# Performance work log

Hardware: AMD Instinct MI355X
Metric: run time of the kernel (lower is better)

## Reference

```python
import jax, jax.numpy as jnp
import numpy as np

B, T, H = 2, 2048, 1024
NH = 16
HD = H // NH


def setup_inputs() -> dict:
    key = jax.random.key(0)
    ks = jax.random.split(key, 9)
    s = 0.02
    return {
        "x": jax.random.normal(ks[0], (B, T, H), dtype=jnp.float32),
        "attn_mask": jnp.ones((B, T), dtype=jnp.int32),
        "Wq": jax.random.normal(ks[1], (H, H), dtype=jnp.float32) * s,
        "bq": jnp.zeros((H,), dtype=jnp.float32),
        "Wk": jax.random.normal(ks[2], (H, H), dtype=jnp.float32) * s,
        "bk": jnp.zeros((H,), dtype=jnp.float32),
        "Wv": jax.random.normal(ks[3], (H, H), dtype=jnp.float32) * s,
        "bv": jnp.zeros((H,), dtype=jnp.float32),
        "Wo": jax.random.normal(ks[4], (H, H), dtype=jnp.float32) * s,
        "bo": jnp.zeros((H,), dtype=jnp.float32),
    }


def reference(x, attn_mask, Wq, bq, Wk, bk, Wv, bv, Wo, bo):
    Bc, Tc, Hc = x.shape
    scale = HD ** -0.5
    # projections; torch Linear: y = x @ W.T + b (here W stored as [in,out])
    q = (x @ Wq + bq).reshape(Bc, Tc, NH, HD).transpose(0, 2, 1, 3)  # [B,NH,T,HD]
    k = (x @ Wk + bk).reshape(Bc, Tc, NH, HD).transpose(0, 2, 1, 3)
    v = (x @ Wv + bv).reshape(Bc, Tc, NH, HD).transpose(0, 2, 1, 3)
    scores = jnp.einsum('bhqd,bhkd->bhqk', q, k) * scale  # [B,NH,T,T]
    mask = attn_mask.reshape(Bc, 1, 1, Tc)
    scores = jnp.where(mask == 0, jnp.float32(-jnp.inf), scores)
    probs = jax.nn.softmax(scores, axis=-1)
    ctx = jnp.einsum('bhqk,bhkd->bhqd', probs, v)  # [B,NH,T,HD]
    ctx = ctx.transpose(0, 2, 1, 3).reshape(Bc, Tc, Hc)
    out = ctx @ Wo + bo
    return out
```

## Files before the change

kernel.cpp:

```cpp
#include <hip/hip_runtime.h>

typedef _Float16 f16;
typedef _Float16 f16x8 __attribute__((ext_vector_type(8)));
typedef _Float16 f16x4 __attribute__((ext_vector_type(4)));
typedef __fp16 h16x2 __attribute__((ext_vector_type(2)));
typedef float f32x4 __attribute__((ext_vector_type(4)));

#define MFMA32(a, b, c) __builtin_amdgcn_mfma_f32_16x16x32_f16((a), (b), (c), 0, 0, 0)
#define MFMA16(a, b, c) __builtin_amdgcn_mfma_f32_16x16x16f16((a), (b), (c), 0, 0, 0)

static constexpr int Bb = 2, T = 2048, H = 1024, NH = 16, HD = 64;
static constexpr int M = Bb * T;
static constexpr int NQKV = 3 * H;
#define QSCALE 0.1803368801111f

__device__ __forceinline__ void gload_lds16(const void* g, void* l) {
  __builtin_amdgcn_global_load_lds(
      (const __attribute__((address_space(1))) void*)g,
      (__attribute__((address_space(3))) void*)l, 16, 0, 0);
}

__global__ __launch_bounds__(256) void pack_all(const float* __restrict__ x,
                                                const float* __restrict__ Wq,
                                                const float* __restrict__ Wk,
                                                const float* __restrict__ Wv,
                                                const float* __restrict__ Wo,
                                                const float* __restrict__ bq,
                                                const float* __restrict__ bk,
                                                const float* __restrict__ bv,
                                                f16* __restrict__ xh,
                                                f16* __restrict__ WqkvT,
                                                f16* __restrict__ WoT,
                                                float* __restrict__ bqkv) {
  __shared__ f16 tile[64][65];
  const int bid = blockIdx.x;
  if (bid < 4096) {
    int i = bid * 256 + threadIdx.x;
    float4 v = ((const float4*)x)[i];
    f16x4 o;
    o[0] = (f16)v.x; o[1] = (f16)v.y; o[2] = (f16)v.z; o[3] = (f16)v.w;
    *(f16x4*)(xh + (size_t)i * 4) = o;
  } else if (bid < 5120) {
    int t = bid - 4096;
    int z = t >> 8, rem = t & 255;
    const float* W = (z == 0) ? Wq : (z == 1) ? Wk : (z == 2) ? Wv : Wo;
    f16* Wt = (z < 3) ? (WqkvT + (size_t)z * H * H) : WoT;
    const float scale = (z == 0) ? QSCALE : 1.0f;
    int k0 = (rem >> 4) * 64, n0 = (rem & 15) * 64;
    for (int p = 0; p < 16; ++p) {
      int idx = threadIdx.x + p * 256;
      int r = idx >> 6, c = idx & 63;
      tile[r][c] = (f16)(W[(size_t)(k0 + r) * H + n0 + c] * scale);
    }
    __syncthreads();
    for (int p = 0; p < 16; ++p) {
      int idx = threadIdx.x + p * 256;
      int r = idx >> 6, c = idx & 63;
      Wt[(size_t)(n0 + r) * H + k0 + c] = tile[c][r];
    }
  } else {
    int i = (bid - 5120) * 256 + threadIdx.x;
    if (i < 3072) {
      float v = (i < 1024) ? bq[i] * QSCALE : ((i < 2048) ? bk[i - 1024] : bv[i - 2048]);
      bqkv[i] = v;
    }
  }
}

__device__ __forceinline__ f16x8 lds_frag(const f16* base, int row, int gr) {
  return *(const f16x8*)(base + row * 64 + ((gr ^ (row & 7)) << 3));
}

template <int TM, int TN, bool OUT_F32>
__global__ __launch_bounds__(256) void gemm_f16_bt(const f16* __restrict__ A,
                                                   const f16* __restrict__ Bt,
                                                   const float* __restrict__ bias,
                                                   void* __restrict__ Cout,
                                                   int Nn, int Kk) {
  __shared__ f16 As[TM * 64];
  __shared__ f16 Bs[TN * 64];
  const int tid = threadIdx.x;
  const int lane = tid & 63, w = tid >> 6;
  const int quad = lane >> 4, l16 = lane & 15;
  const int wm = w >> 1, wn = w & 1;
  const int m0 = blockIdx.y * TM, n0 = blockIdx.x * TN;
  constexpr int AM = TM / 32, AN = TN / 32;

  f32x4 acc[AM][AN];
  for (int a = 0; a < AM; ++a)
    for (int b2 = 0; b2 < AN; ++b2)
      for (int r = 0; r < 4; ++r) acc[a][b2][r] = 0.f;

  for (int k0 = 0; k0 < Kk; k0 += 64) {
    for (int p = 0; p < TM * 8 / 256; ++p) {
      int slot = p * 256 + w * 64 + lane;
      int r = slot >> 3, g = (slot & 7) ^ (r & 7);
      gload_lds16(A + (size_t)(m0 + r) * Kk + k0 + g * 8,
                  (char*)As + (p * 256 + w * 64) * 16);
    }
    for (int p = 0; p < TN * 8 / 256; ++p) {
      int slot = p * 256 + w * 64 + lane;
      int r = slot >> 3, g = (slot & 7) ^ (r & 7);
      gload_lds16(Bt + (size_t)(n0 + r) * Kk + k0 + g * 8,
                  (char*)Bs + (p * 256 + w * 64) * 16);
    }
    __syncthreads();
    for (int ks = 0; ks < 2; ++ks) {
      f16x8 af[AM], bf[AN];
      for (int t = 0; t < AM; ++t)
        af[t] = lds_frag(As, wm * (TM / 2) + t * 16 + l16, ks * 4 + quad);
      for (int t = 0; t < AN; ++t)
        bf[t] = lds_frag(Bs, wn * (TN / 2) + t * 16 + l16, ks * 4 + quad);
      for (int tm = 0; tm < AM; ++tm)
        for (int tn = 0; tn < AN; ++tn)
          acc[tm][tn] = MFMA32(af[tm], bf[tn], acc[tm][tn]);
    }
    __syncthreads();
  }

  for (int tm = 0; tm < AM; ++tm)
    for (int tn = 0; tn < AN; ++tn)
      for (int r = 0; r < 4; ++r) {
        int m = m0 + wm * (TM / 2) + tm * 16 + quad * 4 + r;
        int n = n0 + wn * (TN / 2) + tn * 16 + l16;
        float v = acc[tm][tn][r] + bias[n];
        if (OUT_F32)
          ((float*)Cout)[(size_t)m * Nn + n] = v;
        else
          ((f16*)Cout)[(size_t)m * Nn + n] = (f16)v;
      }
}


__global__ __launch_bounds__(256) void attn_fused(const f16* __restrict__ QKV,
                                                  const int* __restrict__ mask,
                                                  f16* __restrict__ ctx) {
  __shared__ f16 Kt[2][128 * 64];
  __shared__ f16 Vt[2][80 * 128];

  const int tid = threadIdx.x;
  const int w = tid >> 6, lane = tid & 63;
  const int quad = lane >> 4, l16 = lane & 15;
  const int q0 = blockIdx.x * 128, h = blockIdx.y, b = blockIdx.z;

  const int vkv = tid & 127;
  const int vgb = (tid >> 7) * 4;
  const size_t kbase = (size_t)(b * T) * NQKV + H + h * HD;
  const size_t vbase = (size_t)(b * T) * NQKV + 2 * H + h * HD;

  f16x8 qf[2][2];
  for (int tq = 0; tq < 2; ++tq) {
    const f16* qrow = QKV + (size_t)(b * T + q0 + w * 32 + tq * 16 + l16) * NQKV + h * HD;
    qf[tq][0] = *(const f16x8*)(qrow + quad * 8);
    qf[tq][1] = *(const f16x8*)(qrow + 32 + quad * 8);
  }

  f32x4 oacc[2][5];
  for (int tq = 0; tq < 2; ++tq)
    for (int t = 0; t < 5; ++t)
      for (int r = 0; r < 4; ++r) oacc[tq][t][r] = 0.f;

  for (int p = 0; p < 4; ++p) {
    int slot = p * 256 + w * 64 + lane;
    int r = slot >> 3, g = (slot & 7) ^ (r & 7);
    gload_lds16(QKV + kbase + (size_t)r * NQKV + g * 8,
                (char*)&Kt[0][0] + (p * 256 + w * 64) * 16);
  }
  {
    f16 vm = (f16)(float)(mask[b * T + vkv] != 0);
    const f16* vrow = QKV + vbase + (size_t)vkv * NQKV;
    for (int p = 0; p < 4; ++p) {
      int g = vgb + p;
      f16x8 v = *(const f16x8*)(vrow + g * 8);
      for (int j = 0; j < 8; ++j) {
        int d = g * 8 + j;
        Vt[0][d * 128 + ((vkv + 4 * (d & 15)) & 127)] = v[j] * vm;
      }
    }
    if (tid < 128) Vt[0][64 * 128 + vkv] = vm;
  }
  __syncthreads();

  for (int it = 0; it < T / 128; ++it) {
    const int cur = it & 1, nxt = cur ^ 1;
    const int kvn = (it + 1) * 128;
    const bool pf = kvn < T;

    f16x8 vreg[4] = {};
    f16 vm = (f16)0;
    if (pf) {
      for (int p = 0; p < 4; ++p) {
        int slot = p * 256 + w * 64 + lane;
        int r = slot >> 3, g = (slot & 7) ^ (r & 7);
        gload_lds16(QKV + kbase + (size_t)(kvn + r) * NQKV + g * 8,
                    (char*)&Kt[nxt][0] + (p * 256 + w * 64) * 16);
      }
      vm = (f16)(float)(mask[b * T + kvn + vkv] != 0);
      const f16* vrow = QKV + vbase + (size_t)(kvn + vkv) * NQKV;
      for (int p = 0; p < 4; ++p)
        vreg[p] = *(const f16x8*)(vrow + (vgb + p) * 8);
    }

    const f16* Kc = &Kt[cur][0];
    const f16* Vc = &Vt[cur][0];
    for (int tk = 0; tk < 8; ++tk) {
      f16x8 kf0 = lds_frag(Kc, tk * 16 + l16, quad);
      f16x8 kf1 = lds_frag(Kc, tk * 16 + l16, 4 + quad);
      f16x4 vf[5];
      for (int td = 0; td < 5; ++td)
        vf[td] = *(const f16x4*)&Vc[(td * 16 + l16) * 128 +
                                    ((tk * 16 + quad * 4 + 4 * l16) & 127)];
      for (int tq = 0; tq < 2; ++tq) {
        f32x4 s = {0.f, 0.f, 0.f, 0.f};
        s = MFMA32(kf0, qf[tq][0], s);
        s = MFMA32(kf1, qf[tq][1], s);
        h16x2 p01 = __builtin_amdgcn_cvt_pkrtz(__builtin_amdgcn_exp2f(s[0]),
                                               __builtin_amdgcn_exp2f(s[1]));
        h16x2 p23 = __builtin_amdgcn_cvt_pkrtz(__builtin_amdgcn_exp2f(s[2]),
                                               __builtin_amdgcn_exp2f(s[3]));
        f16x4 pfr;
        pfr[0] = (f16)p01[0]; pfr[1] = (f16)p01[1];
        pfr[2] = (f16)p23[0]; pfr[3] = (f16)p23[1];
        for (int td = 0; td < 5; ++td)
          oacc[tq][td] = MFMA16(vf[td], pfr, oacc[tq][td]);
      }
    }

    if (pf) {
      for (int p = 0; p < 4; ++p) {
        int g = vgb + p;
        for (int j = 0; j < 8; ++j) {
          int d = g * 8 + j;
          Vt[nxt][d * 128 + (((kvn + vkv) + 4 * (d & 15)) & 127)] = vreg[p][j] * vm;
        }
      }
      if (tid < 128) Vt[nxt][64 * 128 + vkv] = vm;
      __syncthreads();
    }
  }

  for (int tq = 0; tq < 2; ++tq) {
    float lq = __shfl(oacc[tq][4][0], l16, 64);
    float inv = 1.f / lq;
    int row = b * T + q0 + w * 32 + tq * 16 + l16;
    for (int td = 0; td < 4; ++td) {
      f16x4 o;
      for (int r = 0; r < 4; ++r) o[r] = (f16)(oacc[tq][td][r] * inv);
      *(f16x4*)(ctx + (size_t)row * H + h * HD + td * 16 + quad * 4) = o;
    }
  }
}


extern "C" void kernel_launch(void* const* d_in, const int* in_sizes, int n_in,
                              void* d_out, int out_size, void* d_ws, size_t ws_size,
                              hipStream_t stream) {
  const float* x  = (const float*)d_in[0];
  const int* mask = (const int*)d_in[1];
  const float* Wq = (const float*)d_in[2];
  const float* bq = (const float*)d_in[3];
  const float* Wk = (const float*)d_in[4];
  const float* bk = (const float*)d_in[5];
  const float* Wv = (const float*)d_in[6];
  const float* bv = (const float*)d_in[7];
  const float* Wo = (const float*)d_in[8];
  const float* bo = (const float*)d_in[9];
  float* out = (float*)d_out;

  char* ws = (char*)d_ws;
  f16* xh      = (f16*)(ws);
  f16* Wqkv_t  = (f16*)(ws + (8u  << 20));
  f16* Wot     = (f16*)(ws + (14u << 20));
  float* bqkv  = (float*)(ws + (16u << 20));
  f16* QKV     = (f16*)(ws + (17u << 20));
  f16* ctx     = (f16*)(ws + (42u << 20));

  pack_all<<<dim3(5132), 256, 0, stream>>>(x, Wq, Wk, Wv, Wo, bq, bk, bv,
                                           xh, Wqkv_t, Wot, bqkv);

  gemm_f16_bt<128, 128, false><<<dim3(NQKV / 128, M / 128), 256, 0, stream>>>(
      xh, Wqkv_t, bqkv, QKV, NQKV, H);

  attn_fused<<<dim3(T / 128, NH, Bb), 256, 0, stream>>>(QKV, mask, ctx);

  gemm_f16_bt<128, 64, true><<<dim3(H / 64, M / 128), 256, 0, stream>>>(
      ctx, Wot, bo, out, H, H);
}
```

Before: 212.1 us.

## Split attention KV across two wave groups with pre-transposed V and async loads

Adds a separate kernel that transposes V into a [B,NH,HD,T] layout so the attention kernel can load V tiles into LDS with async global-to-LDS copies, instead of transposing through registers each iteration. The attention block grows to 512 threads, and two wave groups split each 128-key tile, with their partial outputs combined through LDS at the end. The PV product moves to the 16x16x32 MFMA. The mask is pre-converted to float and multiplied into the probabilities, with the row sum kept in registers instead of through an extra V column. This adds a kernel launch, extra global traffic for the transposed V, and a final cross-group reduction.

New measurement: 209.9 us. No clear change (-1.1%).

```diff
diff --git a/kernel.cpp b/kernel.cpp
--- a/kernel.cpp
+++ b/kernel.cpp
@@ -7,7 +7,6 @@
 typedef float f32x4 __attribute__((ext_vector_type(4)));
 
 #define MFMA32(a, b, c) __builtin_amdgcn_mfma_f32_16x16x32_f16((a), (b), (c), 0, 0, 0)
-#define MFMA16(a, b, c) __builtin_amdgcn_mfma_f32_16x16x16f16((a), (b), (c), 0, 0, 0)
 
 static constexpr int Bb = 2, T = 2048, H = 1024, NH = 16, HD = 64;
 static constexpr int M = Bb * T;
@@ -28,10 +27,12 @@
                                                 const float* __restrict__ bq,
                                                 const float* __restrict__ bk,
                                                 const float* __restrict__ bv,
+                                                const int* __restrict__ mask,
                                                 f16* __restrict__ xh,
                                                 f16* __restrict__ WqkvT,
                                                 f16* __restrict__ WoT,
-                                                float* __restrict__ bqkv) {
+                                                float* __restrict__ bqkv,
+                                                float* __restrict__ maskf) {
   __shared__ f16 tile[64][65];
   const int bid = blockIdx.x;
   if (bid < 4096) {
@@ -58,12 +59,40 @@
       int r = idx >> 6, c = idx & 63;
       Wt[(size_t)(n0 + r) * H + k0 + c] = tile[c][r];
     }
-  } else {
+  } else if (bid < 5132) {
     int i = (bid - 5120) * 256 + threadIdx.x;
     if (i < 3072) {
       float v = (i < 1024) ? bq[i] * QSCALE : ((i < 2048) ? bk[i - 1024] : bv[i - 2048]);
       bqkv[i] = v;
     }
+  } else {
+    int i = (bid - 5132) * 256 + threadIdx.x;
+    if (i < Bb * T) maskf[i] = mask[i] ? 1.0f : 0.0f;
+  }
+}
+
+__global__ __launch_bounds__(256) void vtrans(const f16* __restrict__ QKV,
+                                              f16* __restrict__ VT) {
+  __shared__ f16 tile[64 * 64];
+  const int tid = threadIdx.x;
+  const int kv0 = blockIdx.x * 64, h = blockIdx.y, b = blockIdx.z;
+  for (int p = 0; p < 2; ++p) {
+    int idx = p * 256 + tid;
+    int r = idx >> 3, gr = idx & 7;
+    f16x8 v = *(const f16x8*)(QKV + (size_t)(b * T + kv0 + r) * NQKV + 2 * H + h * HD + gr * 8);
+    *(f16x8*)&tile[r * 64 + (((gr + (r >> 3)) & 7) << 3)] = v;
+  }
+  __syncthreads();
+  const size_t obase = ((size_t)(b * NH + h) * HD) * T + kv0;
+  for (int p = 0; p < 2; ++p) {
+    int idx = p * 256 + tid;
+    int d = idx >> 3, kg = idx & 7;
+    f16x8 v;
+    for (int j = 0; j < 8; ++j) {
+      int row = kg * 8 + j;
+      v[j] = tile[row * 64 + ((((d >> 3) + kg) & 7) << 3) + (d & 7)];
+    }
+    *(f16x8*)(VT + obase + (size_t)d * T + kg * 8) = v;
   }
 }
 
@@ -132,121 +161,141 @@
 }
 
 
-__global__ __launch_bounds__(256) void attn_fused(const f16* __restrict__ QKV,
-                                                  const int* __restrict__ mask,
-                                                  f16* __restrict__ ctx) {
-  __shared__ f16 Kt[2][128 * 64];
-  __shared__ f16 Vt[2][80 * 128];
+static constexpr int KT_ELE = 128 * 64;
+static constexpr int VT_ELE = 64 * 128;
+
+__global__ __launch_bounds__(512, 4) void attn_fused(const f16* __restrict__ QKV,
+                                                     const f16* __restrict__ VT,
+                                                     const float* __restrict__ maskf,
+                                                     f16* __restrict__ ctx) {
+  __shared__ char smem[(2 * KT_ELE + 2 * VT_ELE) * 2];
+  f16* KtB = (f16*)smem;
+  f16* VtB = (f16*)(smem + 2 * KT_ELE * 2);
 
   const int tid = threadIdx.x;
   const int w = tid >> 6, lane = tid & 63;
   const int quad = lane >> 4, l16 = lane & 15;
+  const int qw = w & 3, g = w >> 2;
   const int q0 = blockIdx.x * 128, h = blockIdx.y, b = blockIdx.z;
 
-  const int vkv = tid & 127;
-  const int vgb = (tid >> 7) * 4;
   const size_t kbase = (size_t)(b * T) * NQKV + H + h * HD;
-  const size_t vbase = (size_t)(b * T) * NQKV + 2 * H + h * HD;
+  const size_t vtbase = ((size_t)(b * NH + h) * HD) * T;
+  const float* maskp = maskf + b * T;
 
   f16x8 qf[2][2];
   for (int tq = 0; tq < 2; ++tq) {
-    const f16* qrow = QKV + (size_t)(b * T + q0 + w * 32 + tq * 16 + l16) * NQKV + h * HD;
+    const f16* qrow = QKV + (size_t)(b * T + q0 + qw * 32 + tq * 16 + l16) * NQKV + h * HD;
     qf[tq][0] = *(const f16x8*)(qrow + quad * 8);
     qf[tq][1] = *(const f16x8*)(qrow + 32 + quad * 8);
   }
 
-  f32x4 oacc[2][5];
+  f32x4 oacc[2][4];
+  float lsum[2] = {0.f, 0.f};
   for (int tq = 0; tq < 2; ++tq)
-    for (int t = 0; t < 5; ++t)
+    for (int t = 0; t < 4; ++t)
       for (int r = 0; r < 4; ++r) oacc[tq][t][r] = 0.f;
 
-  for (int p = 0; p < 4; ++p) {
-    int slot = p * 256 + w * 64 + lane;
-    int r = slot >> 3, g = (slot & 7) ^ (r & 7);
-    gload_lds16(QKV + kbase + (size_t)r * NQKV + g * 8,
-                (char*)&Kt[0][0] + (p * 256 + w * 64) * 16);
-  }
-  {
-    f16 vm = (f16)(float)(mask[b * T + vkv] != 0);
-    const f16* vrow = QKV + vbase + (size_t)vkv * NQKV;
-    for (int p = 0; p < 4; ++p) {
-      int g = vgb + p;
-      f16x8 v = *(const f16x8*)(vrow + g * 8);
-      for (int j = 0; j < 8; ++j) {
-        int d = g * 8 + j;
-        Vt[0][d * 128 + ((vkv + 4 * (d & 15)) & 127)] = v[j] * vm;
-      }
-    }
-    if (tid < 128) Vt[0][64 * 128 + vkv] = vm;
-  }
+  auto stage = [&](int kv0, int buf) {
+    f16* Kd = KtB + buf * KT_ELE;
+    f16* Vd = VtB + buf * VT_ELE;
+    for (int p = 0; p < 2; ++p) {
+      int s = p * 512 + tid;
+      int R = s >> 3, sg = (s & 7) ^ (R & 7);
+      int kv = (R & ~31) | ((R & 12) << 1) | ((R & 16) >> 2) | (R & 3);
+      gload_lds16(QKV + kbase + (size_t)(kv0 + kv) * NQKV + sg * 8,
+                  (char*)Kd + (p * 512 + w * 64) * 16);
+    }
+    for (int p = 0; p < 2; ++p) {
+      int s = p * 512 + tid;
+      int d = s >> 4, cg = s & 15;
+      int kvl = (cg * 8 - 8 * (d & 15)) & 127;
+      gload_lds16(VT + vtbase + (size_t)d * T + kv0 + kvl,
+                  (char*)Vd + (p * 512 + w * 64) * 16);
+    }
+  };
+
+  stage(0, 0);
   __syncthreads();
 
   for (int it = 0; it < T / 128; ++it) {
     const int cur = it & 1, nxt = cur ^ 1;
-    const int kvn = (it + 1) * 128;
-    const bool pf = kvn < T;
-
-    f16x8 vreg[4] = {};
-    f16 vm = (f16)0;
-    if (pf) {
-      for (int p = 0; p < 4; ++p) {
-        int slot = p * 256 + w * 64 + lane;
-        int r = slot >> 3, g = (slot & 7) ^ (r & 7);
-        gload_lds16(QKV + kbase + (size_t)(kvn + r) * NQKV + g * 8,
-                    (char*)&Kt[nxt][0] + (p * 256 + w * 64) * 16);
+    if (it + 1 < T / 128) stage((it + 1) * 128, nxt);
+
+    const f16* Kc = KtB + cur * KT_ELE;
+    const f16* Vc = VtB + cur * VT_ELE;
+
+    for (int s = 0; s < 2; ++s) {
+      const int bi = g * 2 + s;
+      const int kvabs = it * 128 + bi * 32;
+      float4 m0 = *(const float4*)(maskp + kvabs + quad * 8);
+      float4 m1 = *(const float4*)(maskp + kvabs + quad * 8 + 4);
+      f16x8 kfA0 = lds_frag(Kc, bi * 32 + l16, quad);
+      f16x8 kfA1 = lds_frag(Kc, bi * 32 + l16, 4 + quad);
+      f16x8 kfB0 = lds_frag(Kc, bi * 32 + 16 + l16, quad);
+      f16x8 kfB1 = lds_frag(Kc, bi * 32 + 16 + l16, 4 + quad);
+      f16x8 vf[4];
+      for (int td = 0; td < 4; ++td)
+        vf[td] = *(const f16x8*)&Vc[(td * 16 + l16) * 128 +
+                                    ((bi * 32 + quad * 8 + 8 * l16) & 127)];
+      for (int tq = 0; tq < 2; ++tq) {
+        f32x4 sA = {0.f, 0.f, 0.f, 0.f}, sB = {0.f, 0.f, 0.f, 0.f};
+        sA = MFMA32(kfA0, qf[tq][0], sA);
+        sA = MFMA32(kfA1, qf[tq][1], sA);
+        sB = MFMA32(kfB0, qf[tq][0], sB);
+        sB = MFMA32(kfB1, qf[tq][1], sB);
+        float pA0 = __builtin_amdgcn_exp2f(sA[0]) * m0.x;
+        float pA1 = __builtin_amdgcn_exp2f(sA[1]) * m0.y;
+        float pA2 = __builtin_amdgcn_exp2f(sA[2]) * m0.z;
+        float pA3 = __builtin_amdgcn_exp2f(sA[3]) * m0.w;
+        float pB0 = __builtin_amdgcn_exp2f(sB[0]) * m1.x;
+        float pB1 = __builtin_amdgcn_exp2f(sB[1]) * m1.y;
+        float pB2 = __builtin_amdgcn_exp2f(sB[2]) * m1.z;
+        float pB3 = __builtin_amdgcn_exp2f(sB[3]) * m1.w;
+        lsum[tq] += ((pA0 + pA1) + (pA2 + pA3)) + ((pB0 + pB1) + (pB2 + pB3));
+        union PF { f16x8 v; h16x2 h[4]; } pf;
+        pf.h[0] = __builtin_amdgcn_cvt_pkrtz(pA0, pA1);
+        pf.h[1] = __builtin_amdgcn_cvt_pkrtz(pA2, pA3);
+        pf.h[2] = __builtin_amdgcn_cvt_pkrtz(pB0, pB1);
+        pf.h[3] = __builtin_amdgcn_cvt_pkrtz(pB2, pB3);
+        for (int td = 0; td < 4; ++td)
+          oacc[tq][td] = MFMA32(vf[td], pf.v, oacc[tq][td]);
       }
-      vm = (f16)(float)(mask[b * T + kvn + vkv] != 0);
-      const f16* vrow = QKV + vbase + (size_t)(kvn + vkv) * NQKV;
-      for (int p = 0; p < 4; ++p)
-        vreg[p] = *(const f16x8*)(vrow + (vgb + p) * 8);
-    }
-
-    const f16* Kc = &Kt[cur][0];
-    const f16* Vc = &Vt[cur][0];
-    for (int tk = 0; tk < 8; ++tk) {
-      f16x8 kf0 = lds_frag(Kc, tk * 16 + l16, quad);
-      f16x8 kf1 = lds_frag(Kc, tk * 16 + l16, 4 + quad);
-      f16x4 vf[5];
-      for (int td = 0; td < 5; ++td)
-        vf[td] = *(const f16x4*)&Vc[(td * 16 + l16) * 128 +
-                                    ((tk * 16 + quad * 4 + 4 * l16) & 127)];
-      for (int tq = 0; tq < 2; ++tq) {
-        f32x4 s = {0.f, 0.f, 0.f, 0.f};
-        s = MFMA32(kf0, qf[tq][0], s);
-        s = MFMA32(kf1, qf[tq][1], s);
-        h16x2 p01 = __builtin_amdgcn_cvt_pkrtz(__builtin_amdgcn_exp2f(s[0]),
-                                               __builtin_amdgcn_exp2f(s[1]));
-        h16x2 p23 = __builtin_amdgcn_cvt_pkrtz(__builtin_amdgcn_exp2f(s[2]),
-                                               __builtin_amdgcn_exp2f(s[3]));
-        f16x4 pfr;
-        pfr[0] = (f16)p01[0]; pfr[1] = (f16)p01[1];
-        pfr[2] = (f16)p23[0]; pfr[3] = (f16)p23[1];
-        for (int td = 0; td < 5; ++td)
-          oacc[tq][td] = MFMA16(vf[td], pfr, oacc[tq][td]);
+    }
+    __syncthreads();
+  }
+
+  float* cmb = (float*)smem;
+  const int slot = qw * 64 + lane;
+  if (g == 1) {
+    float* dst = cmb + slot * 35;
+    int i = 0;
+    for (int tq = 0; tq < 2; ++tq)
+      for (int td = 0; td < 4; ++td)
+        for (int r = 0; r < 4; ++r) dst[i++] = oacc[tq][td][r];
+    dst[32] = lsum[0];
+    dst[33] = lsum[1];
+  }
+  __syncthreads();
+  if (g == 0) {
+    const float* src = cmb + slot * 35;
+    int i = 0;
+    for (int tq = 0; tq < 2; ++tq)
+      for (int td = 0; td < 4; ++td)
+        for (int r = 0; r < 4; ++r) oacc[tq][td][r] += src[i++];
+    lsum[0] += src[32];
+    lsum[1] += src[33];
+
+    for (int tq = 0; tq < 2; ++tq) {
+      float l = lsum[tq];
+      l += __shfl_xor(l, 16, 64);
+      l += __shfl_xor(l, 32, 64);
+      float inv = 1.f / l;
+      int row = b * T + q0 + qw * 32 + tq * 16 + l16;
+      for (int td = 0; td < 4; ++td) {
+        f16x4 o;
+        for (int r = 0; r < 4; ++r) o[r] = (f16)(oacc[tq][td][r] * inv);
+        *(f16x4*)(ctx + (size_t)row * H + h * HD + td * 16 + quad * 4) = o;
       }
-    }
-
-    if (pf) {
-      for (int p = 0; p < 4; ++p) {
-        int g = vgb + p;
-        for (int j = 0; j < 8; ++j) {
-          int d = g * 8 + j;
-          Vt[nxt][d * 128 + (((kvn + vkv) + 4 * (d & 15)) & 127)] = vreg[p][j] * vm;
-        }
-      }
-      if (tid < 128) Vt[nxt][64 * 128 + vkv] = vm;
-      __syncthreads();
-    }
-  }
-
-  for (int tq = 0; tq < 2; ++tq) {
-    float lq = __shfl(oacc[tq][4][0], l16, 64);
-    float inv = 1.f / lq;
-    int row = b * T + q0 + w * 32 + tq * 16 + l16;
-    for (int td = 0; td < 4; ++td) {
-      f16x4 o;
-      for (int r = 0; r < 4; ++r) o[r] = (f16)(oacc[tq][td][r] * inv);
-      *(f16x4*)(ctx + (size_t)row * H + h * HD + td * 16 + quad * 4) = o;
     }
   }
 }
@@ -272,16 +321,20 @@
   f16* Wqkv_t  = (f16*)(ws + (8u  << 20));
   f16* Wot     = (f16*)(ws + (14u << 20));
   float* bqkv  = (float*)(ws + (16u << 20));
+  float* maskf = (float*)(ws + (16u << 20) + 65536);
   f16* QKV     = (f16*)(ws + (17u << 20));
   f16* ctx     = (f16*)(ws + (42u << 20));
-
-  pack_all<<<dim3(5132), 256, 0, stream>>>(x, Wq, Wk, Wv, Wo, bq, bk, bv,
-                                           xh, Wqkv_t, Wot, bqkv);
+  f16* VTr     = (f16*)(ws + (50u << 20));
+
+  pack_all<<<dim3(5164), 256, 0, stream>>>(x, Wq, Wk, Wv, Wo, bq, bk, bv, mask,
+                                           xh, Wqkv_t, Wot, bqkv, maskf);
 
   gemm_f16_bt<128, 128, false><<<dim3(NQKV / 128, M / 128), 256, 0, stream>>>(
       xh, Wqkv_t, bqkv, QKV, NQKV, H);
 
-  attn_fused<<<dim3(T / 128, NH, Bb), 256, 0, stream>>>(QKV, mask, ctx);
+  vtrans<<<dim3(T / 64, NH, Bb), 256, 0, stream>>>(QKV, VTr);
+
+  attn_fused<<<dim3(T / 128, NH, Bb), 512, 0, stream>>>(QKV, VTr, maskf, ctx);
 
   gemm_f16_bt<128, 64, true><<<dim3(H / 64, M / 128), 256, 0, stream>>>(
       ctx, Wot, bo, out, H, H);
```
